# Kernel optimization log

Hardware: AMD Instinct MI355X
Metric: run time of the kernel (lower is better)

The kernel has to match this reference:

```python
import math
import jax, jax.numpy as jnp
import numpy as np

B, S, H = 4, 2048, 1024

def setup_inputs() -> dict:
    key = jax.random.key(0)
    ks = jax.random.split(key, 7)
    scale = 1.0 / math.sqrt(H)
    return {
        "X":  jax.random.normal(ks[0], (B, S, H), dtype=jnp.float32),
        "Wq": jax.random.normal(ks[1], (H, H), dtype=jnp.float32) * scale,
        "bq": jnp.zeros((H,), dtype=jnp.float32),
        "Wk": jax.random.normal(ks[2], (H, H), dtype=jnp.float32) * scale,
        "bk": jnp.zeros((H,), dtype=jnp.float32),
        "Wv": jax.random.normal(ks[3], (H, H), dtype=jnp.float32) * scale,
        "bv": jnp.zeros((H,), dtype=jnp.float32),
    }

def reference(X, Wq, bq, Wk, bk, Wv, bv):
    # nn.Linear: y = x @ W.T + b
    Q = jnp.einsum("bsh,oh->bso", X, Wq) + bq
    K = jnp.einsum("bsh,oh->bso", X, Wk) + bk
    V = jnp.einsum("bsh,oh->bso", X, Wv) + bv
    hidden_dim = X.shape[-1]
    scores = jnp.einsum("bqh,bkh->bqk", Q, K) / jnp.sqrt(jnp.float32(hidden_dim))
    attn = jax.nn.softmax(scores, axis=-1)  # [B, S, S]
    return jnp.einsum("bqk,bkh->bqh", attn, V)
```

## Files before the change

### kernel.cpp

```cpp
#include <hip/hip_runtime.h>
#include <stdint.h>

#define ASG __attribute__((address_space(1)))
#define ASL __attribute__((address_space(3)))

typedef __bf16 bf16x8 __attribute__((ext_vector_type(8)));
typedef float f32x4 __attribute__((ext_vector_type(4)));

__device__ __forceinline__ unsigned short f2bf(float f) {
  unsigned int u = __builtin_bit_cast(unsigned int, f);
  u = (u + 0x7fffu + ((u >> 16) & 1u)) >> 16;
  return (unsigned short)u;
}

__global__ __launch_bounds__(256) void k_prep(
    const float* __restrict__ X, const float* __restrict__ Wq,
    const float* __restrict__ Wk, const float* __restrict__ Wv,
    const float* __restrict__ bq, const float* __restrict__ bk,
    const float* __restrict__ bv,
    unsigned short* __restrict__ Xb, float* __restrict__ biasF) {
  const int bid = blockIdx.x, tid = threadIdx.x;
  unsigned short* Wb = Xb + 8388608;
  if (bid < 11264) {
    const float* src;
    ushort4* dst;
    int j;
    if (bid < 8192) {
      j = bid * 256 + tid; src = X; dst = (ushort4*)Xb;
    } else {
      int w = (bid - 8192) >> 10;
      j = ((bid - 8192) & 1023) * 256 + tid;
      src = (w == 0) ? Wq : (w == 1 ? Wk : Wv);
      dst = (ushort4*)(Wb + (long)w * 1048576);
    }
    float4 v = reinterpret_cast<const float4*>(src)[j];
    ushort4 o;
    o.x = f2bf(v.x); o.y = f2bf(v.y); o.z = f2bf(v.z); o.w = f2bf(v.w);
    dst[j] = o;
  } else {
    int i = (bid - 11264) * 256 + tid;
    if (i < 3072)
      biasF[i] = (i < 1024) ? bq[i] : (i < 2048 ? bk[i - 1024] : bv[i - 2048]);
  }
}

template <int OUT_MODE, int BIAS>
__global__ __launch_bounds__(512, 2) void gemm3r(
    const unsigned short* __restrict__ A, const unsigned short* __restrict__ B,
    void* __restrict__ Cv, const float* __restrict__ bias,
    int lda, int ldb, int ldc, int K, float alpha,
    long sA, long sB, long sC) {
  __shared__ __align__(16) char smem[147456];
  const int tid = threadIdx.x;
  const int wid = tid >> 6, lane = tid & 63;
  const int wr = wid >> 2, wc = wid & 3;
  const int bm0 = blockIdx.y << 7, bn0 = blockIdx.x << 8;
  A += (long)blockIdx.z * sA;
  B += (long)blockIdx.z * sB;
  const int NT = K >> 6;

  const int srow = tid >> 3;
  const int scol = (((tid & 7) ^ (srow & 7)) << 3);
  long gA[2], gB[4];
#pragma unroll
  for (int u = 0; u < 2; ++u)
    gA[u] = (long)(bm0 + u * 64 + srow) * lda + scol;
#pragma unroll
  for (int u = 0; u < 4; ++u)
    gB[u] = (long)(bn0 + u * 64 + srow) * ldb + scol;

#define STG(PTR, GOFF, KK, LDSOFF)                                             \
  __builtin_amdgcn_global_load_lds((ASG const void*)((PTR) + (GOFF) + ((KK) << 6)), \
      (ASL void*)(smem + (LDSOFF) + wid * 1024), 16, 0, 0)

#define STG_P1(KK, SB_) do { int kk = (KK); if (kk >= NT) kk -= NT;            \
    STG(A, gA[0], kk, (SB_));                                                  \
    STG(A, gA[1], kk, (SB_) + 8192);                                           \
    STG(B, gB[0], kk, (SB_) + 16384); } while (0)
#define STG_P2(KK, SB_) do { int kk = (KK); if (kk >= NT) kk -= NT;            \
    STG(B, gB[1], kk, (SB_) + 24576);                                          \
    STG(B, gB[2], kk, (SB_) + 32768);                                          \
    STG(B, gB[3], kk, (SB_) + 40960); } while (0)

  const int arow0 = (wr * 64 + (lane & 15)) << 7;
  const int brow0 = 16384 + ((wc * 64 + (lane & 15)) << 7);
  int colk[2];
#pragma unroll
  for (int ks = 0; ks < 2; ++ks)
    colk[ks] = (((ks << 2) + (lane >> 4)) ^ (lane & 7)) << 4;

  bf16x8 afr[4][2];
  bf16x8 b01[2][2];
  bf16x8 b23[2][2];
  f32x4 acc[4][4] = {};

#define RDA(CB) do { _Pragma("unroll") for (int mf = 0; mf < 4; ++mf)          \
    _Pragma("unroll") for (int ks = 0; ks < 2; ++ks)                           \
      afr[mf][ks] = *(const bf16x8*)(smem + (CB) + arow0 + (mf << 11) + colk[ks]); } while (0)
#define RDB01(CB) do { _Pragma("unroll") for (int nf = 0; nf < 2; ++nf)        \
    _Pragma("unroll") for (int ks = 0; ks < 2; ++ks)                           \
      b01[nf][ks] = *(const bf16x8*)(smem + (CB) + brow0 + (nf << 11) + colk[ks]); } while (0)
#define RDB23(CB) do { _Pragma("unroll") for (int nf = 0; nf < 2; ++nf)        \
    _Pragma("unroll") for (int ks = 0; ks < 2; ++ks)                           \
      b23[nf][ks] = *(const bf16x8*)(smem + (CB) + brow0 + ((nf + 2) << 11) + colk[ks]); } while (0)

#define MM(BF, NB) do { __builtin_amdgcn_s_setprio(1);                         \
    _Pragma("unroll") for (int mf = 0; mf < 4; ++mf)                           \
    _Pragma("unroll") for (int nf = 0; nf < 2; ++nf)                           \
    _Pragma("unroll") for (int ks = 0; ks < 2; ++ks)                           \
      acc[mf][(NB) + nf] = __builtin_amdgcn_mfma_f32_16x16x32_bf16(            \
          afr[mf][ks], BF[nf][ks], acc[mf][(NB) + nf], 0, 0, 0);               \
    __builtin_amdgcn_s_setprio(0); } while (0)

  STG_P1(0, 0); STG_P2(0, 0);
  STG_P1(1, 49152); STG_P2(1, 49152);
  asm volatile("s_waitcnt vmcnt(6)" ::: "memory");
  __builtin_amdgcn_s_barrier();

  int bc = 0, bs = 2 * 49152;
  for (int t = 0; t < NT; ++t) {
    RDA(bc); RDB01(bc);
    STG_P1(t + 2, bs);
    __builtin_amdgcn_s_barrier();
    asm volatile("s_waitcnt lgkmcnt(0)" ::: "memory");
    __builtin_amdgcn_sched_barrier(0);
    MM(b01, 0);
    __builtin_amdgcn_sched_barrier(0);
    __builtin_amdgcn_s_barrier();
    RDB23(bc);
    STG_P2(t + 2, bs);
    __builtin_amdgcn_s_barrier();
    asm volatile("s_waitcnt lgkmcnt(0)" ::: "memory");
    __builtin_amdgcn_sched_barrier(0);
    MM(b23, 2);
    __builtin_amdgcn_sched_barrier(0);
    asm volatile("s_waitcnt vmcnt(6)" ::: "memory");
    __builtin_amdgcn_s_barrier();
    bc += 49152; if (bc == 147456) bc = 0;
    bs += 49152; if (bs == 147456) bs = 0;
  }

  const int r0 = bm0 + wr * 64 + ((lane >> 4) << 2);
  const int c0 = bn0 + wc * 64 + (lane & 15);
#pragma unroll
  for (int mf = 0; mf < 4; ++mf)
#pragma unroll
    for (int nf = 0; nf < 4; ++nf) {
      const int row0 = r0 + mf * 16;
      const int col = c0 + nf * 16;
      f32x4 v = acc[mf][nf];
      const float bb = BIAS ? bias[col] : 0.0f;
      if (OUT_MODE == 0) {
        unsigned short* C = (unsigned short*)Cv + (long)blockIdx.z * sC;
#pragma unroll
        for (int j = 0; j < 4; ++j)
          C[(long)(row0 + j) * ldc + col] = f2bf(v[j] * alpha + bb);
      } else {
        float* C = (float*)Cv + (long)blockIdx.z * sC;
#pragma unroll
        for (int j = 0; j < 4; ++j)
          C[(long)(row0 + j) * ldc + col] = v[j] * alpha + bb;
      }
    }
#undef STG
#undef STG_P1
#undef STG_P2
#undef RDA
#undef RDB01
#undef RDB23
#undef MM
}

__global__ __launch_bounds__(256) void k_softmax_bf16(unsigned short* __restrict__ S) {
  long row = blockIdx.x;
  unsigned short* R = S + row * 2048;
  int t = threadIdx.x;
  int wid = t >> 6, lane = t & 63;
  uint4 raw = reinterpret_cast<const uint4*>(R)[t];
  unsigned int w[4] = {raw.x, raw.y, raw.z, raw.w};
  float v[8];
#pragma unroll
  for (int j = 0; j < 4; ++j) {
    v[2 * j]     = __builtin_bit_cast(float, (unsigned int)(w[j] << 16));
    v[2 * j + 1] = __builtin_bit_cast(float, (unsigned int)(w[j] & 0xffff0000u));
  }
  float m = v[0];
#pragma unroll
  for (int j = 1; j < 8; ++j) m = fmaxf(m, v[j]);
#pragma unroll
  for (int off = 32; off >= 1; off >>= 1) m = fmaxf(m, __shfl_xor(m, off));
  __shared__ float red[8];
  if (lane == 0) red[wid] = m;
  __syncthreads();
  m = fmaxf(fmaxf(red[0], red[1]), fmaxf(red[2], red[3]));

  float e[8], s = 0.f;
#pragma unroll
  for (int j = 0; j < 8; ++j) { e[j] = __expf(v[j] - m); s += e[j]; }
#pragma unroll
  for (int off = 32; off >= 1; off >>= 1) s += __shfl_xor(s, off);
  if (lane == 0) red[4 + wid] = s;
  __syncthreads();
  s = red[4] + red[5] + red[6] + red[7];
  float inv = 1.0f / s;

  uint4 o;
  unsigned int* ow = &o.x;
#pragma unroll
  for (int j = 0; j < 4; ++j)
    ow[j] = (unsigned int)f2bf(e[2 * j] * inv) |
            ((unsigned int)f2bf(e[2 * j + 1] * inv) << 16);
  reinterpret_cast<uint4*>(R)[t] = o;
}

__global__ __launch_bounds__(256) void k_transpose_v(const unsigned short* __restrict__ V,
                                                     unsigned short* __restrict__ Vt) {
  __shared__ unsigned short tile[32][33];
  int b = blockIdx.z;
  int s0 = blockIdx.y * 32, h0 = blockIdx.x * 32;
  const unsigned short* Vb = V + (long)b * 2048 * 3072;
  unsigned short* Vtb = Vt + (long)b * 1024 * 2048;
  int tx = threadIdx.x & 31, ty = threadIdx.x >> 5;
#pragma unroll
  for (int i = 0; i < 4; ++i)
    tile[ty + 8 * i][tx] = Vb[(long)(s0 + ty + 8 * i) * 3072 + h0 + tx];
  __syncthreads();
#pragma unroll
  for (int i = 0; i < 4; ++i)
    Vtb[(long)(h0 + ty + 8 * i) * 2048 + s0 + tx] = tile[tx][ty + 8 * i];
}

extern "C" void kernel_launch(void* const* d_in, const int* in_sizes, int n_in,
                              void* d_out, int out_size, void* d_ws, size_t ws_size,
                              hipStream_t stream) {
  const float* X  = (const float*)d_in[0];
  const float* Wq = (const float*)d_in[1];
  const float* bq = (const float*)d_in[2];
  const float* Wk = (const float*)d_in[3];
  const float* bk = (const float*)d_in[4];
  const float* Wv = (const float*)d_in[5];
  const float* bv = (const float*)d_in[6];
  float* out = (float*)d_out;
  (void)in_sizes; (void)n_in; (void)out_size; (void)ws_size;

  constexpr long S = 2048, H = 1024;
  constexpr long MS = 4 * S;

  size_t off = 0;
  auto alloc = [&](size_t bytes) { char* p = (char*)d_ws + off; off += bytes; return p; };
  unsigned short* Xb    = (unsigned short*)alloc(MS * H * 2);
  unsigned short* Wb    = (unsigned short*)alloc(3 * H * H * 2);
  float*          biasF = (float*)alloc(3 * H * 4);
  unsigned short* QKVb  = (unsigned short*)alloc(MS * 3 * H * 2);
  unsigned short* Vt    = (unsigned short*)alloc(4 * H * S * 2);
  unsigned short* Sb    = (unsigned short*)alloc(4 * S * S * 2);
  (void)Wb;

  k_prep<<<dim3(11276), 256, 0, stream>>>(X, Wq, Wk, Wv, bq, bk, bv, Xb, biasF);

  gemm3r<0, 1><<<dim3(12, 64, 1), 512, 0, stream>>>(Xb, Xb + MS * H, QKVb, biasF,
                                                    1024, 1024, 3072, 1024, 1.0f, 0, 0, 0);

  gemm3r<0, 0><<<dim3(8, 16, 4), 512, 0, stream>>>(QKVb, QKVb + 1024, Sb, nullptr,
                                                   3072, 3072, 2048, 1024, 0.03125f,
                                                   S * 3 * H, S * 3 * H, S * S);

  k_softmax_bf16<<<dim3((int)MS), 256, 0, stream>>>(Sb);

  k_transpose_v<<<dim3(32, 64, 4), 256, 0, stream>>>(QKVb + 2048, Vt);

  gemm3r<1, 0><<<dim3(4, 16, 4), 512, 0, stream>>>(Sb, Vt, out, nullptr,
                                                   2048, 2048, 1024, 2048, 1.0f,
                                                   S * S, H * S, S * H);
}
```

Baseline: 175.6 us.

## Restructure GEMM main loop to one barrier per K-step with fragment prefetch

```diff
diff --git a/kernel.cpp b/kernel.cpp
--- a/kernel.cpp
+++ b/kernel.cpp
@@ -45,7 +45,7 @@
 }
 
 template <int OUT_MODE, int BIAS>
-__global__ __launch_bounds__(512, 2) void gemm3r(
+__global__ __launch_bounds__(512, 2) void gemm3p(
     const unsigned short* __restrict__ A, const unsigned short* __restrict__ B,
     void* __restrict__ Cv, const float* __restrict__ bias,
     int lda, int ldb, int ldc, int K, float alpha,
@@ -73,11 +73,10 @@
   __builtin_amdgcn_global_load_lds((ASG const void*)((PTR) + (GOFF) + ((KK) << 6)), \
       (ASL void*)(smem + (LDSOFF) + wid * 1024), 16, 0, 0)
 
-#define STG_P1(KK, SB_) do { int kk = (KK); if (kk >= NT) kk -= NT;            \
+#define STG_ALL(KK, SB_) do { int kk = (KK); if (kk >= NT) kk -= NT;           \
     STG(A, gA[0], kk, (SB_));                                                  \
     STG(A, gA[1], kk, (SB_) + 8192);                                           \
-    STG(B, gB[0], kk, (SB_) + 16384); } while (0)
-#define STG_P2(KK, SB_) do { int kk = (KK); if (kk >= NT) kk -= NT;            \
+    STG(B, gB[0], kk, (SB_) + 16384);                                          \
     STG(B, gB[1], kk, (SB_) + 24576);                                          \
     STG(B, gB[2], kk, (SB_) + 32768);                                          \
     STG(B, gB[3], kk, (SB_) + 40960); } while (0)
@@ -104,40 +103,33 @@
     _Pragma("unroll") for (int ks = 0; ks < 2; ++ks)                           \
       b23[nf][ks] = *(const bf16x8*)(smem + (CB) + brow0 + ((nf + 2) << 11) + colk[ks]); } while (0)
 
-#define MM(BF, NB) do { __builtin_amdgcn_s_setprio(1);                         \
+#define MM(BF, NB) do {                                                        \
     _Pragma("unroll") for (int mf = 0; mf < 4; ++mf)                           \
     _Pragma("unroll") for (int nf = 0; nf < 2; ++nf)                           \
     _Pragma("unroll") for (int ks = 0; ks < 2; ++ks)                           \
       acc[mf][(NB) + nf] = __builtin_amdgcn_mfma_f32_16x16x32_bf16(            \
-          afr[mf][ks], BF[nf][ks], acc[mf][(NB) + nf], 0, 0, 0);               \
-    __builtin_amdgcn_s_setprio(0); } while (0)
-
-  STG_P1(0, 0); STG_P2(0, 0);
-  STG_P1(1, 49152); STG_P2(1, 49152);
+          afr[mf][ks], BF[nf][ks], acc[mf][(NB) + nf], 0, 0, 0); } while (0)
+
+  STG_ALL(0, 0);
+  STG_ALL(1, 49152);
   asm volatile("s_waitcnt vmcnt(6)" ::: "memory");
   __builtin_amdgcn_s_barrier();
+  RDA(0); RDB01(0);
 
   int bc = 0, bs = 2 * 49152;
   for (int t = 0; t < NT; ++t) {
-    RDA(bc); RDB01(bc);
-    STG_P1(t + 2, bs);
+    RDB23(bc);
+    STG_ALL(t + 2, bs);
+    __builtin_amdgcn_s_setprio(1);
+    MM(b01, 0);
+    MM(b23, 2);
+    __builtin_amdgcn_s_setprio(0);
+    asm volatile("s_waitcnt vmcnt(6) lgkmcnt(0)" ::: "memory");
     __builtin_amdgcn_s_barrier();
-    asm volatile("s_waitcnt lgkmcnt(0)" ::: "memory");
-    __builtin_amdgcn_sched_barrier(0);
-    MM(b01, 0);
-    __builtin_amdgcn_sched_barrier(0);
-    __builtin_amdgcn_s_barrier();
-    RDB23(bc);
-    STG_P2(t + 2, bs);
-    __builtin_amdgcn_s_barrier();
-    asm volatile("s_waitcnt lgkmcnt(0)" ::: "memory");
-    __builtin_amdgcn_sched_barrier(0);
-    MM(b23, 2);
-    __builtin_amdgcn_sched_barrier(0);
-    asm volatile("s_waitcnt vmcnt(6)" ::: "memory");
-    __builtin_amdgcn_s_barrier();
-    bc += 49152; if (bc == 147456) bc = 0;
-    bs += 49152; if (bs == 147456) bs = 0;
+    const int bn = (bc == 2 * 49152) ? 0 : bc + 49152;
+    if (t + 1 < NT) { RDA(bn); RDB01(bn); }
+    bc = bn;
+    bs = (bs == 2 * 49152) ? 0 : bs + 49152;
   }
 
   const int r0 = bm0 + wr * 64 + ((lane >> 4) << 2);
@@ -163,8 +155,7 @@
       }
     }
 #undef STG
-#undef STG_P1
-#undef STG_P2
+#undef STG_ALL
 #undef RDA
 #undef RDB01
 #undef RDB23
@@ -258,10 +249,10 @@
 
   k_prep<<<dim3(11276), 256, 0, stream>>>(X, Wq, Wk, Wv, bq, bk, bv, Xb, biasF);
 
-  gemm3r<0, 1><<<dim3(12, 64, 1), 512, 0, stream>>>(Xb, Xb + MS * H, QKVb, biasF,
+  gemm3p<0, 1><<<dim3(12, 64, 1), 512, 0, stream>>>(Xb, Xb + MS * H, QKVb, biasF,
                                                     1024, 1024, 3072, 1024, 1.0f, 0, 0, 0);
 
-  gemm3r<0, 0><<<dim3(8, 16, 4), 512, 0, stream>>>(QKVb, QKVb + 1024, Sb, nullptr,
+  gemm3p<0, 0><<<dim3(8, 16, 4), 512, 0, stream>>>(QKVb, QKVb + 1024, Sb, nullptr,
                                                    3072, 3072, 2048, 1024, 0.03125f,
                                                    S * 3 * H, S * 3 * H, S * S);
 
@@ -269,7 +260,7 @@
 
   k_transpose_v<<<dim3(32, 64, 4), 256, 0, stream>>>(QKVb + 2048, Vt);
 
-  gemm3r<1, 0><<<dim3(4, 16, 4), 512, 0, stream>>>(Sb, Vt, out, nullptr,
+  gemm3p<1, 0><<<dim3(4, 16, 4), 512, 0, stream>>>(Sb, Vt, out, nullptr,
                                                    2048, 2048, 1024, 2048, 1.0f,
                                                    S * S, H * S, S * H);
 }
```

Measured after the change: 170.0 us. 3.2% less time.
